# Optimization experiments

Measured on AMD Instinct MI355X. Metric: run time of the kernel, lower is better.

The kernel has to match this reference:

```python
import jax, jax.numpy as jnp
import numpy as np

N_STREAMS = 4
HIDDEN = 1024
SINKHORN_ITERS = 20
TAU = 0.05
EPS = 1e-6
RMS_EPS = 1e-8


def rms_norm(x, weight):
    # x: [T, d] fp32
    rms = jnp.mean(x * x, axis=-1, keepdims=True)
    return x * jax.lax.rsqrt(rms + RMS_EPS) * weight


def sinkhorn_log(logits, n_iters=SINKHORN_ITERS, tau=TAU):
    # logits: [T, n, n] -> doubly-stochastic [T, n, n]
    Z = logits / tau
    u0 = jnp.zeros(Z.shape[:-1], Z.dtype)  # [T, n]
    v0 = jnp.zeros_like(u0)

    def body(i, uv):
        u, v = uv
        u = -jax.nn.logsumexp(Z + v[..., None, :], axis=-1)
        v = -jax.nn.logsumexp(Z + u[..., :, None], axis=-2)
        return (u, v)

    u, v = jax.lax.fori_loop(0, n_iters, body, (u0, v0))
    return jnp.exp(Z + u[..., :, None] + v[..., None, :])


def setup_inputs() -> dict:
    key = jax.random.key(0)
    ks = jax.random.split(key, 6)
    d = N_STREAMS * HIDDEN
    x_streams = jax.random.normal(ks[0], (4, 2048, N_STREAMS, HIDDEN), dtype=jnp.float32)
    scale = 1.0 / np.sqrt(d)
    return {
        "x_streams": x_streams,
        "rms_weight": jnp.ones((d,), jnp.float32),
        "W_pre": jax.random.normal(ks[1], (N_STREAMS, d), jnp.float32) * scale,
        "W_post": jax.random.normal(ks[2], (N_STREAMS, d), jnp.float32) * scale,
        "W_res": jax.random.normal(ks[3], (N_STREAMS * N_STREAMS, d), jnp.float32) * scale,
        "bias_pre": jnp.zeros((N_STREAMS,), jnp.float32),
        "bias_post": jnp.zeros((N_STREAMS,), jnp.float32),
        "bias_res": jnp.zeros((N_STREAMS * N_STREAMS,), jnp.float32),
        "alpha_pre": jnp.full((1,), 0.01, jnp.float32),
        "alpha_post": jnp.full((1,), 0.01, jnp.float32),
        "alpha_res": jnp.full((1,), 0.01, jnp.float32),
        "W_sub": jax.random.normal(ks[4], (HIDDEN, HIDDEN), jnp.float32) * (1.0 / np.sqrt(HIDDEN)),
    }


def reference(x_streams, rms_weight, W_pre, W_post, W_res, bias_pre, bias_post,
              bias_res, alpha_pre, alpha_post, alpha_res, W_sub):
    B, S, n, C = x_streams.shape
    d = n * C
    x_flat = x_streams.reshape(B * S, d).astype(jnp.float32)
    x_norm = rms_norm(x_flat, rms_weight)

    H_pre = jax.nn.sigmoid(alpha_pre * (x_norm @ W_pre.T) + bias_pre)        # [T, n]
    H_post = 2.0 * jax.nn.sigmoid(alpha_post * (x_norm @ W_post.T) + bias_post)
    H_res = sinkhorn_log((alpha_res * (x_norm @ W_res.T) + bias_res).reshape(B * S, n, n))

    H_pre = H_pre.reshape(B, S, n)
    H_post = H_post.reshape(B, S, n)
    H_res = H_res.reshape(B, S, n, n)

    H_pre_w = H_pre / (jnp.sum(H_pre, axis=-1, keepdims=True) + EPS)
    H_post_w = H_post / (jnp.sum(H_post, axis=-1, keepdims=True) + EPS)

    # pre-aggregate streams -> single stream
    x_layer = jnp.einsum('bsnc,bsn->bsc', x_streams, H_pre_w)
    # sublayer: bias-free linear
    y = x_layer @ W_sub.T                                                    # [B, S, C]
    # broadcast sublayer output back to streams
    y_expanded = H_post_w[..., None] * y[:, :, None, :]                      # [B, S, n, C]
    # doubly-stochastic residual stream mixing
    x_mixed = jnp.einsum('bsic,bsoi->bsoc', x_streams, H_res)
    return x_mixed + y_expanded
```

## Files before the change

kernel.cpp:

```cpp
#include <hip/hip_runtime.h>

#define NTOK 8192
#define D 4096
#define CH 1024

typedef __attribute__((ext_vector_type(8))) short short8v;
typedef __attribute__((ext_vector_type(4))) float float4v;
typedef __attribute__((ext_vector_type(4))) unsigned short ushort4v;

static __device__ __forceinline__ unsigned short f2bf(float f) {
  unsigned int u = __float_as_uint(f);
  u += 0x7fff + ((u >> 16) & 1);
  return (unsigned short)(u >> 16);
}

static __device__ __forceinline__ float bf2f(unsigned short u) {
  return __uint_as_float(((unsigned int)u) << 16);
}

static __device__ __forceinline__ void async_cp16(const void* g, void* l) {
  __builtin_amdgcn_global_load_lds((__attribute__((address_space(1))) void*)g,
                                   (__attribute__((address_space(3))) void*)l,
                                   16, 0, 0);
}

__global__ __launch_bounds__(512, 4) void gates_kernel(
    const float* __restrict__ x, const float* __restrict__ rms_w,
    const float* __restrict__ Wpre, const float* __restrict__ Wpost,
    const float* __restrict__ Wres, const float* __restrict__ bpre,
    const float* __restrict__ bpost, const float* __restrict__ bres,
    const float* __restrict__ apre, const float* __restrict__ apost,
    const float* __restrict__ ares, const float* __restrict__ Wsub,
    unsigned short* __restrict__ Wb, float* __restrict__ gates_out,
    unsigned short* __restrict__ xlayer) {
  __shared__ unsigned short xb[8][4096];
  __shared__ float logits_lds[8][24];
  __shared__ float sq_lds[8];
  __shared__ float s_lds[8];
  __shared__ float hpre_lds[8][4];

  const int tid = threadIdx.x;
  const int lane = tid & 63;
  const int w = tid >> 6;
  const int tok0 = blockIdx.x * 8;

  {
    int i = blockIdx.x * 1024 + tid * 2;
    float2 v = *(const float2*)(Wsub + i);
    unsigned int packed = (unsigned int)f2bf(v.x) | ((unsigned int)f2bf(v.y) << 16);
    *(unsigned int*)(Wb + i) = packed;
  }

  {
    const float* src = x + (size_t)(tok0 + w) * D + lane * 4;
    float sq = 0.f;
#pragma unroll
    for (int j = 0; j < 16; ++j) {
      float4 v = *(const float4*)(src + j * 256);
      sq += v.x * v.x + v.y * v.y + v.z * v.z + v.w * v.w;
      uint2 p;
      p.x = (unsigned int)f2bf(v.x) | ((unsigned int)f2bf(v.y) << 16);
      p.y = (unsigned int)f2bf(v.z) | ((unsigned int)f2bf(v.w) << 16);
      *(uint2*)(&xb[w][j * 256 + lane * 4]) = p;
    }
    for (int off = 32; off > 0; off >>= 1) sq += __shfl_xor(sq, off, 64);
    if (lane == 0) sq_lds[w] = sq;
  }

  const float* Wp[3];
#pragma unroll
  for (int g = 0; g < 3; ++g) {
    int gg = w * 3 + g;
    Wp[g] = (gg < 4) ? (Wpre + gg * D)
          : (gg < 8) ? (Wpost + (gg - 4) * D)
                     : (Wres + (gg - 8) * D);
  }

  float acc[3][8];
#pragma unroll
  for (int g = 0; g < 3; ++g)
#pragma unroll
    for (int t = 0; t < 8; ++t) acc[g][t] = 0.f;

  __syncthreads();

#pragma unroll 4
  for (int chk = 0; chk < 16; ++chk) {
    const int cb = chk * 256 + lane * 4;
    float4 r4 = *(const float4*)(rms_w + cb);
    float4 wr[3];
#pragma unroll
    for (int g = 0; g < 3; ++g) {
      float4 w4 = *(const float4*)(Wp[g] + cb);
      wr[g].x = w4.x * r4.x; wr[g].y = w4.y * r4.y;
      wr[g].z = w4.z * r4.z; wr[g].w = w4.w * r4.w;
    }
#pragma unroll
    for (int t = 0; t < 8; ++t) {
      ushort4v xv = *(const ushort4v*)(&xb[t][cb]);
      float x0 = bf2f(xv.x), x1 = bf2f(xv.y), x2 = bf2f(xv.z), x3 = bf2f(xv.w);
#pragma unroll
      for (int g = 0; g < 3; ++g)
        acc[g][t] += x0 * wr[g].x + x1 * wr[g].y + x2 * wr[g].z + x3 * wr[g].w;
    }
  }

#pragma unroll
  for (int g = 0; g < 3; ++g)
#pragma unroll
    for (int t = 0; t < 8; ++t) {
      float v = acc[g][t];
      for (int off = 32; off > 0; off >>= 1) v += __shfl_xor(v, off, 64);
      if (lane == 0) logits_lds[t][w * 3 + g] = v;
    }
  __syncthreads();

  if (tid < 8) {
    const int t = tid;
    float s = rsqrtf(sq_lds[t] * (1.0f / 4096.0f) + 1e-8f);
    s_lds[t] = s;
    float a_pre = apre[0], a_post = apost[0];

    float hp[4];
    float sum_p = 1e-6f;
#pragma unroll
    for (int i = 0; i < 4; ++i) {
      float z = a_pre * (s * logits_lds[t][i]) + bpre[i];
      hp[i] = 1.0f / (1.0f + __expf(-z));
      sum_p += hp[i];
    }
    float inv_p = 1.0f / sum_p;
#pragma unroll
    for (int i = 0; i < 4; ++i) hpre_lds[t][i] = hp[i] * inv_p;

    float* go = gates_out + (size_t)(tok0 + t) * 20;
    float hq[4];
    float sum_q = 1e-6f;
#pragma unroll
    for (int i = 0; i < 4; ++i) {
      float z = a_post * (s * logits_lds[t][4 + i]) + bpost[i];
      hq[i] = 2.0f / (1.0f + __expf(-z));
      sum_q += hq[i];
    }
    float inv_q = 1.0f / sum_q;
#pragma unroll
    for (int i = 0; i < 4; ++i) go[i] = hq[i] * inv_q;
  }
  __syncthreads();

  auto phB = [&](int sI) {
    const int t = sI >> 8;
    const int c4 = (sI & 255) * 4;
    const float h0 = hpre_lds[t][0], h1 = hpre_lds[t][1];
    const float h2 = hpre_lds[t][2], h3 = hpre_lds[t][3];
    ushort4v v0 = *(const ushort4v*)&xb[t][c4];
    ushort4v v1 = *(const ushort4v*)&xb[t][1024 + c4];
    ushort4v v2 = *(const ushort4v*)&xb[t][2048 + c4];
    ushort4v v3 = *(const ushort4v*)&xb[t][3072 + c4];
    ushort4v o;
    o.x = f2bf(h0 * bf2f(v0.x) + h1 * bf2f(v1.x) + h2 * bf2f(v2.x) + h3 * bf2f(v3.x));
    o.y = f2bf(h0 * bf2f(v0.y) + h1 * bf2f(v1.y) + h2 * bf2f(v2.y) + h3 * bf2f(v3.y));
    o.z = f2bf(h0 * bf2f(v0.z) + h1 * bf2f(v1.z) + h2 * bf2f(v2.z) + h3 * bf2f(v3.z));
    o.w = f2bf(h0 * bf2f(v0.w) + h1 * bf2f(v1.w) + h2 * bf2f(v2.w) + h3 * bf2f(v3.w));
    *(ushort4v*)(xlayer + (size_t)(tok0 + t) * CH + c4) = o;
  };

  if (w == 0) {
    if (lane < 32) {
      const int t = lane >> 2;
      const int r = lane & 3;
      const float s = s_lds[t];
      const float a_res = ares[0];
      float Zrow[4], Zcol[4];
#pragma unroll
      for (int j = 0; j < 4; ++j) {
        Zrow[j] = (a_res * (s * logits_lds[t][8 + r * 4 + j]) + bres[r * 4 + j]) * 20.0f;
        Zcol[j] = (a_res * (s * logits_lds[t][8 + j * 4 + r]) + bres[j * 4 + r]) * 20.0f;
      }
      float u = 0.f, v = 0.f;
      const int base = t << 2;
      for (int it = 0; it < 20; ++it) {
        float v0 = __shfl(v, base + 0, 64), v1 = __shfl(v, base + 1, 64);
        float v2 = __shfl(v, base + 2, 64), v3 = __shfl(v, base + 3, 64);
        float a0 = Zrow[0] + v0, a1 = Zrow[1] + v1, a2 = Zrow[2] + v2, a3 = Zrow[3] + v3;
        float m = fmaxf(fmaxf(a0, a1), fmaxf(a2, a3));
        float sm = __expf(a0 - m) + __expf(a1 - m) + __expf(a2 - m) + __expf(a3 - m);
        u = -(m + __logf(sm));
        float u0 = __shfl(u, base + 0, 64), u1 = __shfl(u, base + 1, 64);
        float u2 = __shfl(u, base + 2, 64), u3 = __shfl(u, base + 3, 64);
        float b0 = Zcol[0] + u0, b1 = Zcol[1] + u1, b2 = Zcol[2] + u2, b3 = Zcol[3] + u3;
        float m2 = fmaxf(fmaxf(b0, b1), fmaxf(b2, b3));
        float sm2 = __expf(b0 - m2) + __expf(b1 - m2) + __expf(b2 - m2) + __expf(b3 - m2);
        v = -(m2 + __logf(sm2));
      }
      float v0 = __shfl(v, base + 0, 64), v1 = __shfl(v, base + 1, 64);
      float v2 = __shfl(v, base + 2, 64), v3 = __shfl(v, base + 3, 64);
      float* go = gates_out + (size_t)(tok0 + t) * 20;
      go[4 + r * 4 + 0] = __expf(Zrow[0] + u + v0);
      go[4 + r * 4 + 1] = __expf(Zrow[1] + u + v1);
      go[4 + r * 4 + 2] = __expf(Zrow[2] + u + v2);
      go[4 + r * 4 + 3] = __expf(Zrow[3] + u + v3);
    }
#pragma unroll
    for (int i = 0; i < 4; ++i) phB(1792 + i * 64 + lane);
  } else {
    const int b = tid - 64;
#pragma unroll
    for (int i = 0; i < 4; ++i) phB(b + i * 448);
  }
}

__global__ __launch_bounds__(256, 2) void gemm_epi(
    const unsigned short* __restrict__ A,
    const unsigned short* __restrict__ B,
    const float* __restrict__ x,
    const float* __restrict__ gates,
    float* __restrict__ out) {
  __shared__ __align__(16) unsigned short stg[32768];
  __shared__ float hpost_sm[128][4];
  __shared__ float hres_sm[128][16];

  const int tid = threadIdx.x;
  const int lane = tid & 63;
  const int w = tid >> 6;
  const int n0 = blockIdx.x * 128;
  const int m0 = blockIdx.y * 128;

  {
    const int r = tid >> 1, half = tid & 1;
    const float* gp = gates + (size_t)(m0 + r) * 20 + half * 10;
#pragma unroll
    for (int j = 0; j < 10; ++j) {
      int jj = half * 10 + j;
      float v = gp[j];
      if (jj < 4) hpost_sm[r][jj] = v;
      else        hres_sm[r][jj - 4] = v;
    }
  }

  float4v accf[4][4];
#pragma unroll
  for (int mi = 0; mi < 4; ++mi)
#pragma unroll
    for (int ni = 0; ni < 4; ++ni) {
      accf[mi][ni].x = 0.f; accf[mi][ni].y = 0.f;
      accf[mi][ni].z = 0.f; accf[mi][ni].w = 0.f;
    }

  const int wm = (w >> 1) * 64;
  const int wn = (w & 1) * 64;
  const int srow = lane >> 3;
  const int sslot = lane & 7;

#define STAGE(KT, BUF)                                                        \
  {                                                                           \
    const int k0s = (KT) * 64;                                                \
    unsigned short* As = stg + (BUF) * 8192;                                  \
    unsigned short* Bs = stg + 16384 + (BUF) * 8192;                          \
    _Pragma("unroll")                                                         \
    for (int i = 0; i < 4; ++i) {                                             \
      int chunk = w * 4 + i;                                                  \
      int row = chunk * 8 + srow;                                             \
      int qg = sslot ^ (row & 7);                                             \
      async_cp16(A + (size_t)(m0 + row) * 1024 + k0s + qg * 8,                \
                 (void*)(As + chunk * 512));                                  \
      async_cp16(B + (size_t)(n0 + row) * 1024 + k0s + qg * 8,                \
                 (void*)(Bs + chunk * 512));                                  \
    }                                                                         \
  }

  STAGE(0, 0);
  __syncthreads();

  for (int kt = 0; kt < 16; ++kt) {
    const int cur = kt & 1;
    if (kt < 15) STAGE(kt + 1, cur ^ 1);
    const unsigned short* As = stg + cur * 8192;
    const unsigned short* Bs = stg + 16384 + cur * 8192;
#pragma unroll
    for (int kk = 0; kk < 2; ++kk) {
      short8v a[4], b[4];
#pragma unroll
      for (int mi = 0; mi < 4; ++mi) {
        int row = wm + mi * 16 + (lane & 15);
        int q = (kk * 4 + (lane >> 4)) ^ (row & 7);
        a[mi] = *(const short8v*)(As + row * 64 + q * 8);
      }
#pragma unroll
      for (int ni = 0; ni < 4; ++ni) {
        int row = wn + ni * 16 + (lane & 15);
        int q = (kk * 4 + (lane >> 4)) ^ (row & 7);
        b[ni] = *(const short8v*)(Bs + row * 64 + q * 8);
      }
#pragma unroll
      for (int mi = 0; mi < 4; ++mi)
#pragma unroll
        for (int ni = 0; ni < 4; ++ni)
          accf[mi][ni] = __builtin_amdgcn_mfma_f32_16x16x32_bf16(
              a[mi], b[ni], accf[mi][ni], 0, 0, 0);
    }
    __syncthreads();
  }

  const int rg = (lane >> 4) * 4;
  const int cl = lane & 15;
#pragma unroll
  for (int mi = 0; mi < 4; ++mi) {
#pragma unroll
    for (int r = 0; r < 4; ++r) {
      const int row = wm + mi * 16 + rg + r;
      const size_t t = (size_t)(m0 + row);
      const float4 hq = *(const float4*)(&hpost_sm[row][0]);
      const float4 h0 = *(const float4*)(&hres_sm[row][0]);
      const float4 h1 = *(const float4*)(&hres_sm[row][4]);
      const float4 h2 = *(const float4*)(&hres_sm[row][8]);
      const float4 h3 = *(const float4*)(&hres_sm[row][12]);
      const float* xp = x + t * 4096 + n0 + wn + cl;
      float* op = out + t * 4096 + n0 + wn + cl;
#pragma unroll
      for (int ni = 0; ni < 4; ++ni) {
        const int c = ni * 16;
        float x0 = xp[c], x1 = xp[c + 1024], x2 = xp[c + 2048], x3 = xp[c + 3072];
        float y = accf[mi][ni][r];
        op[c]        = x0 * h0.x + x1 * h0.y + x2 * h0.z + x3 * h0.w + hq.x * y;
        op[c + 1024] = x0 * h1.x + x1 * h1.y + x2 * h1.z + x3 * h1.w + hq.y * y;
        op[c + 2048] = x0 * h2.x + x1 * h2.y + x2 * h2.z + x3 * h2.w + hq.z * y;
        op[c + 3072] = x0 * h3.x + x1 * h3.y + x2 * h3.z + x3 * h3.w + hq.w * y;
      }
    }
  }
}

extern "C" void kernel_launch(void* const* d_in, const int* in_sizes, int n_in,
                              void* d_out, int out_size, void* d_ws, size_t ws_size,
                              hipStream_t stream) {
  const float* x     = (const float*)d_in[0];
  const float* rms_w = (const float*)d_in[1];
  const float* Wpre  = (const float*)d_in[2];
  const float* Wpost = (const float*)d_in[3];
  const float* Wres  = (const float*)d_in[4];
  const float* bpre  = (const float*)d_in[5];
  const float* bpost = (const float*)d_in[6];
  const float* bres  = (const float*)d_in[7];
  const float* apre  = (const float*)d_in[8];
  const float* apost = (const float*)d_in[9];
  const float* ares  = (const float*)d_in[10];
  const float* Wsub  = (const float*)d_in[11];
  float* out = (float*)d_out;

  char* ws = (char*)d_ws;
  float* gates           = (float*)ws;
  unsigned short* Wb     = (unsigned short*)(ws + (1 << 20));
  unsigned short* xlayer = (unsigned short*)(ws + (4 << 20));

  gates_kernel<<<1024, 512, 0, stream>>>(x, rms_w, Wpre, Wpost, Wres, bpre,
                                         bpost, bres, apre, apost, ares,
                                         Wsub, Wb, gates, xlayer);
  gemm_epi<<<dim3(8, 64), 256, 0, stream>>>(xlayer, Wb, x, gates, out);
}
```

Before: 362.8 us.

## Compute gate logits with bf16 MFMA using prefolded weights from prep kernel

Adds a prep kernel that converts W_sub to bf16 and folds rms_weight into the 24 gate weight rows, padding them to 32 and storing them as bf16. The gates kernel then computes the token-by-gate logits with 16x16x32 bf16 MFMA instead of scalar FMAs. It also changes the x staging so each wave covers a K slice of all 8 tokens, with XOR-swizzled LDS writes, and reduces the per-wave partial logits and sums of squares through LDS. The aim is to cut the scalar FMA work and the repeated fp32 weight loads in the gating pass. In exchange it adds one kernel launch and rounds the gate weights to bf16.

```diff
diff --git a/kernel.cpp b/kernel.cpp
--- a/kernel.cpp
+++ b/kernel.cpp
@@ -7,6 +7,7 @@
 typedef __attribute__((ext_vector_type(8))) short short8v;
 typedef __attribute__((ext_vector_type(4))) float float4v;
 typedef __attribute__((ext_vector_type(4))) unsigned short ushort4v;
+typedef __attribute__((ext_vector_type(8))) unsigned short ushort8v;
 
 static __device__ __forceinline__ unsigned short f2bf(float f) {
   unsigned int u = __float_as_uint(f);
@@ -24,17 +25,43 @@
                                    16, 0, 0);
 }
 
+__global__ __launch_bounds__(256) void prep_kernel(
+    const float* __restrict__ Wpre, const float* __restrict__ Wpost,
+    const float* __restrict__ Wres, const float* __restrict__ rms_w,
+    const float* __restrict__ Wsub, unsigned short* __restrict__ Wg,
+    unsigned short* __restrict__ Wb) {
+  const int bid = blockIdx.x;
+  if (bid < 2048) {
+    int i = bid * 512 + threadIdx.x * 2;
+    float2 v = *(const float2*)(Wsub + i);
+    unsigned int packed = (unsigned int)f2bf(v.x) | ((unsigned int)f2bf(v.y) << 16);
+    *(unsigned int*)(Wb + i) = packed;
+  } else {
+    int j = (bid - 2048) * 512 + threadIdx.x * 2;
+    int g = j >> 12;
+    int k = j & 4095;
+    float2 r = *(const float2*)(rms_w + k);
+    float2 wv;
+    if (g < 4)       wv = *(const float2*)(Wpre + g * 4096 + k);
+    else if (g < 8)  wv = *(const float2*)(Wpost + (g - 4) * 4096 + k);
+    else if (g < 24) wv = *(const float2*)(Wres + (g - 8) * 4096 + k);
+    else             { wv.x = 0.f; wv.y = 0.f; }
+    unsigned int packed = (unsigned int)f2bf(wv.x * r.x) |
+                          ((unsigned int)f2bf(wv.y * r.y) << 16);
+    *(unsigned int*)(Wg + g * 4096 + k) = packed;
+  }
+}
+
 __global__ __launch_bounds__(512, 4) void gates_kernel(
-    const float* __restrict__ x, const float* __restrict__ rms_w,
-    const float* __restrict__ Wpre, const float* __restrict__ Wpost,
-    const float* __restrict__ Wres, const float* __restrict__ bpre,
-    const float* __restrict__ bpost, const float* __restrict__ bres,
-    const float* __restrict__ apre, const float* __restrict__ apost,
-    const float* __restrict__ ares, const float* __restrict__ Wsub,
-    unsigned short* __restrict__ Wb, float* __restrict__ gates_out,
-    unsigned short* __restrict__ xlayer) {
-  __shared__ unsigned short xb[8][4096];
-  __shared__ float logits_lds[8][24];
+    const float* __restrict__ x, const unsigned short* __restrict__ Wg,
+    const float* __restrict__ bpre, const float* __restrict__ bpost,
+    const float* __restrict__ bres, const float* __restrict__ apre,
+    const float* __restrict__ apost, const float* __restrict__ ares,
+    float* __restrict__ gates_out, unsigned short* __restrict__ xlayer) {
+  __shared__ __align__(16) unsigned short xb[8][4096];
+  __shared__ float pl[8][8][32];
+  __shared__ float sqp[8][8];
+  __shared__ float logits_lds[8][32];
   __shared__ float sq_lds[8];
   __shared__ float s_lds[8];
   __shared__ float hpre_lds[8][4];
@@ -45,74 +72,72 @@
   const int tok0 = blockIdx.x * 8;
 
   {
-    int i = blockIdx.x * 1024 + tid * 2;
-    float2 v = *(const float2*)(Wsub + i);
-    unsigned int packed = (unsigned int)f2bf(v.x) | ((unsigned int)f2bf(v.y) << 16);
-    *(unsigned int*)(Wb + i) = packed;
-  }
-
+    float sqw[8];
+    const float* src0 = x + (size_t)tok0 * D + w * 512 + lane * 8;
+    const int gslot = w * 64 + lane;
+#pragma unroll
+    for (int t = 0; t < 8; ++t) {
+      const float* s = src0 + (size_t)t * D;
+      float4 a4 = *(const float4*)s;
+      float4 b4 = *(const float4*)(s + 4);
+      sqw[t] = a4.x * a4.x + a4.y * a4.y + a4.z * a4.z + a4.w * a4.w +
+               b4.x * b4.x + b4.y * b4.y + b4.z * b4.z + b4.w * b4.w;
+      ushort8v p;
+      p[0] = f2bf(a4.x); p[1] = f2bf(a4.y); p[2] = f2bf(a4.z); p[3] = f2bf(a4.w);
+      p[4] = f2bf(b4.x); p[5] = f2bf(b4.y); p[6] = f2bf(b4.z); p[7] = f2bf(b4.w);
+      *(ushort8v*)(&xb[t][(gslot ^ t) * 8]) = p;
+    }
+#pragma unroll
+    for (int t = 0; t < 8; ++t) {
+      float v = sqw[t];
+      for (int off = 32; off > 0; off >>= 1) v += __shfl_xor(v, off, 64);
+      if (lane == 0) sqp[w][t] = v;
+    }
+  }
+
+  float4v acc0 = {0.f, 0.f, 0.f, 0.f};
+  float4v acc1 = {0.f, 0.f, 0.f, 0.f};
   {
-    const float* src = x + (size_t)(tok0 + w) * D + lane * 4;
-    float sq = 0.f;
-#pragma unroll
-    for (int j = 0; j < 16; ++j) {
-      float4 v = *(const float4*)(src + j * 256);
-      sq += v.x * v.x + v.y * v.y + v.z * v.z + v.w * v.w;
-      uint2 p;
-      p.x = (unsigned int)f2bf(v.x) | ((unsigned int)f2bf(v.y) << 16);
-      p.y = (unsigned int)f2bf(v.z) | ((unsigned int)f2bf(v.w) << 16);
-      *(uint2*)(&xb[w][j * 256 + lane * 4]) = p;
-    }
-    for (int off = 32; off > 0; off >>= 1) sq += __shfl_xor(sq, off, 64);
-    if (lane == 0) sq_lds[w] = sq;
-  }
-
-  const float* Wp[3];
-#pragma unroll
-  for (int g = 0; g < 3; ++g) {
-    int gg = w * 3 + g;
-    Wp[g] = (gg < 4) ? (Wpre + gg * D)
-          : (gg < 8) ? (Wpost + (gg - 4) * D)
-                     : (Wres + (gg - 8) * D);
-  }
-
-  float acc[3][8];
-#pragma unroll
-  for (int g = 0; g < 3; ++g)
-#pragma unroll
-    for (int t = 0; t < 8; ++t) acc[g][t] = 0.f;
-
+    const int arow = lane & 7;
+    const int apos = lane >> 4;
+    const unsigned short* bb0 =
+        Wg + (size_t)(lane & 15) * D + w * 512 + apos * 8;
+    const unsigned short* bb1 = bb0 + 16 * D;
+#pragma unroll 4
+    for (int ks = 0; ks < 16; ++ks) {
+      short8v a = *(const short8v*)(
+          &xb[arow][((w * 64 + ks * 4 + apos) ^ arow) * 8]);
+      short8v b0 = *(const short8v*)(bb0 + ks * 32);
+      short8v b1 = *(const short8v*)(bb1 + ks * 32);
+      acc0 = __builtin_amdgcn_mfma_f32_16x16x32_bf16(a, b0, acc0, 0, 0, 0);
+      acc1 = __builtin_amdgcn_mfma_f32_16x16x32_bf16(a, b1, acc1, 0, 0, 0);
+    }
+  }
+
+  if (lane < 32) {
+    const int tr = (lane >> 4) * 4;
+    const int gc = lane & 15;
+#pragma unroll
+    for (int r = 0; r < 4; ++r) {
+      pl[w][tr + r][gc] = acc0[r];
+      pl[w][tr + r][16 + gc] = acc1[r];
+    }
+  }
   __syncthreads();
 
-#pragma unroll 4
-  for (int chk = 0; chk < 16; ++chk) {
-    const int cb = chk * 256 + lane * 4;
-    float4 r4 = *(const float4*)(rms_w + cb);
-    float4 wr[3];
-#pragma unroll
-    for (int g = 0; g < 3; ++g) {
-      float4 w4 = *(const float4*)(Wp[g] + cb);
-      wr[g].x = w4.x * r4.x; wr[g].y = w4.y * r4.y;
-      wr[g].z = w4.z * r4.z; wr[g].w = w4.w * r4.w;
-    }
-#pragma unroll
-    for (int t = 0; t < 8; ++t) {
-      ushort4v xv = *(const ushort4v*)(&xb[t][cb]);
-      float x0 = bf2f(xv.x), x1 = bf2f(xv.y), x2 = bf2f(xv.z), x3 = bf2f(xv.w);
-#pragma unroll
-      for (int g = 0; g < 3; ++g)
-        acc[g][t] += x0 * wr[g].x + x1 * wr[g].y + x2 * wr[g].z + x3 * wr[g].w;
-    }
-  }
-
-#pragma unroll
-  for (int g = 0; g < 3; ++g)
-#pragma unroll
-    for (int t = 0; t < 8; ++t) {
-      float v = acc[g][t];
-      for (int off = 32; off > 0; off >>= 1) v += __shfl_xor(v, off, 64);
-      if (lane == 0) logits_lds[t][w * 3 + g] = v;
-    }
+  if (tid < 256) {
+    const int t = tid >> 5, g = tid & 31;
+    float v = 0.f;
+#pragma unroll
+    for (int ww = 0; ww < 8; ++ww) v += pl[ww][t][g];
+    logits_lds[t][g] = v;
+  } else if (tid < 264) {
+    const int t = tid - 256;
+    float v = 0.f;
+#pragma unroll
+    for (int ww = 0; ww < 8; ++ww) v += sqp[ww][t];
+    sq_lds[t] = v;
+  }
   __syncthreads();
 
   if (tid < 8) {
@@ -151,12 +176,14 @@
   auto phB = [&](int sI) {
     const int t = sI >> 8;
     const int c4 = (sI & 255) * 4;
+    const int bi = t * 4096 + (((c4 >> 3) ^ t) << 3) + (c4 & 7);
+    const unsigned short* xr = &xb[0][0];
     const float h0 = hpre_lds[t][0], h1 = hpre_lds[t][1];
     const float h2 = hpre_lds[t][2], h3 = hpre_lds[t][3];
-    ushort4v v0 = *(const ushort4v*)&xb[t][c4];
-    ushort4v v1 = *(const ushort4v*)&xb[t][1024 + c4];
-    ushort4v v2 = *(const ushort4v*)&xb[t][2048 + c4];
-    ushort4v v3 = *(const ushort4v*)&xb[t][3072 + c4];
+    ushort4v v0 = *(const ushort4v*)(xr + bi);
+    ushort4v v1 = *(const ushort4v*)(xr + bi + 1024);
+    ushort4v v2 = *(const ushort4v*)(xr + bi + 2048);
+    ushort4v v3 = *(const ushort4v*)(xr + bi + 3072);
     ushort4v o;
     o.x = f2bf(h0 * bf2f(v0.x) + h1 * bf2f(v1.x) + h2 * bf2f(v2.x) + h3 * bf2f(v3.x));
     o.y = f2bf(h0 * bf2f(v0.y) + h1 * bf2f(v1.y) + h2 * bf2f(v2.y) + h3 * bf2f(v3.y));
@@ -351,10 +378,11 @@
   char* ws = (char*)d_ws;
   float* gates           = (float*)ws;
   unsigned short* Wb     = (unsigned short*)(ws + (1 << 20));
+  unsigned short* Wg     = (unsigned short*)(ws + (3 << 20));
   unsigned short* xlayer = (unsigned short*)(ws + (4 << 20));
 
-  gates_kernel<<<1024, 512, 0, stream>>>(x, rms_w, Wpre, Wpost, Wres, bpre,
-                                         bpost, bres, apre, apost, ares,
-                                         Wsub, Wb, gates, xlayer);
+  prep_kernel<<<2304, 256, 0, stream>>>(Wpre, Wpost, Wres, rms_w, Wsub, Wg, Wb);
+  gates_kernel<<<1024, 512, 0, stream>>>(x, Wg, bpre, bpost, bres,
+                                         apre, apost, ares, gates, xlayer);
   gemm_epi<<<dim3(8, 64), 256, 0, stream>>>(xlayer, Wb, x, gates, out);
 }
```

New measurement: 350.1 us. 1.04x faster.
